# Kernel tuning notes

Hardware: AMD Instinct MI355X
Metric: run time of the kernel (lower is better)

Reference implementation:

```python
import jax, jax.numpy as jnp
import numpy as np

NUM_LEVELS = 16
BASE_RES = 16
DESIRED_RES = 512
EMBED_C = 2
LOG2_HASHMAP = 19
N_POINTS = 262144


def _level_params():
    # torch-ngp gridencoder math, align_corners=True
    S = np.log2(DESIRED_RES / BASE_RES) / (NUM_LEVELS - 1)
    scales = np.exp2(np.arange(NUM_LEVELS) * S) * BASE_RES - 1.0  # float per-level scale
    res = np.ceil(scales).astype(np.int64) + 1                     # per-level grid resolution
    sizes = np.minimum(res ** 3, 2 ** LOG2_HASHMAP)
    sizes = ((sizes + 7) // 8) * 8                                 # round up to multiple of 8
    offsets = np.concatenate([[0], np.cumsum(sizes)])
    return scales.astype(np.float32), res.astype(np.int32), offsets.astype(np.int32)


_CORNERS = np.array([[(c >> d) & 1 for d in range(3)] for c in range(8)], dtype=np.int32)  # [8,3]


def _grid_encode(x, table):
    # x: [N,3] in [0,1]; table: [total_entries, EMBED_C]
    scales, res, offsets = _level_params()
    scales_j = jnp.asarray(scales)[:, None, None]                    # [L,1,1]
    res_j = jnp.asarray(res)[:, None, None]                          # [L,1,1]
    hsize = jnp.asarray(offsets[1:] - offsets[:-1])[:, None, None]   # [L,1,1]
    off = jnp.asarray(offsets[:-1])[:, None, None]                   # [L,1,1]
    pos = x[None, :, :] * scales_j                                   # [L,N,3]
    pos_floor = jnp.floor(pos)
    frac = pos - pos_floor                                           # [L,N,3]
    base = pos_floor.astype(jnp.int32)                               # [L,N,3]
    stride = jnp.concatenate([jnp.ones_like(res_j), res_j, res_j * res_j], axis=-1)  # [L,1,3]
    corners = jnp.asarray(_CORNERS)                                  # [8,3]
    cg = base[:, :, None, :] + corners[None, None]                   # [L,N,8,3]
    w = jnp.where(corners[None, None].astype(bool), frac[:, :, None, :], 1.0 - frac[:, :, None, :])
    w = w[..., 0] * w[..., 1] * w[..., 2]                            # [L,N,8] trilinear weights
    lin = jnp.sum(cg * stride[:, :, None, :], axis=-1)               # [L,N,8] linear corner index
    idx = off + lin % hsize                                          # tiled gridtype: modulo, no hash
    feats = table[idx]                                               # [L,N,8,C] gather
    out = jnp.einsum('lnk,lnkc->lnc', w, feats)                      # [L,N,C]
    n = out.shape[1]
    return out.transpose(1, 0, 2).reshape(n, NUM_LEVELS * EMBED_C)   # [N, L*C]


def setup_inputs() -> dict:
    key = jax.random.key(0)
    ks = jax.random.split(key, 8)
    _, _, offsets = _level_params()
    total = int(offsets[-1])
    inputcoords = jax.random.uniform(ks[0], (N_POINTS, 1, 3), dtype=jnp.float32)  # in [0,1): (x+1)/2 stays in [0,1]
    embeddings = jax.random.normal(ks[1], (total, 1, EMBED_C), dtype=jnp.float32) * 1e-2
    d_in = NUM_LEVELS * EMBED_C  # 32
    W0 = jax.random.normal(ks[2], (d_in, 32), dtype=jnp.float32) / np.sqrt(d_in)
    b0 = jnp.zeros((32,), jnp.float32)
    W1 = jax.random.normal(ks[3], (32, 32), dtype=jnp.float32) / np.sqrt(32.0)
    b1 = jnp.zeros((32,), jnp.float32)
    W2 = jax.random.normal(ks[4], (32, 1), dtype=jnp.float32) / np.sqrt(32.0)
    b2 = jnp.zeros((1,), jnp.float32)
    return {"inputcoords": inputcoords, "embeddings": embeddings,
            "W0": W0, "b0": b0, "W1": W1, "b1": b1, "W2": W2, "b2": b2}


def reference(inputcoords, embeddings, W0, b0, W1, b1, W2, b2):
    bound = 1.0
    x = ((inputcoords + bound) / (2.0 * bound)).reshape(-1, 3)       # [N,3]
    enc = _grid_encode(x, embeddings[:, 0])                          # [N, 32]
    h = enc.reshape(-1, 1, NUM_LEVELS * EMBED_C)                     # [N,1,32]
    h = jax.nn.leaky_relu(h @ W0 + b0, 0.01)
    h = jax.nn.leaky_relu(h @ W1 + b1, 0.01)
    return h @ W2 + b2                                               # [N,1,1]
```

## Files before the change

kernel.cpp:

```cpp
#include <hip/hip_runtime.h>

#define NLVL 16

constexpr float SCALEC[NLVL] = {
    15.0f, 19.15873679831797f, 24.39841683149119f, 31.0f,
    39.31747359663594f, 49.79683366298238f, 63.0f, 79.63494719327189f,
    100.59366732596477f, 127.0f, 160.26989438654376f, 202.18733465192954f,
    255.0f, 321.5397887730875f, 405.3746693038591f, 511.0f
};
constexpr int RESC[NLVL] = {
    16, 21, 26, 32, 41, 51, 64, 81, 102, 128, 162, 204, 256, 323, 407, 512
};
constexpr int OFFC[NLVL] = {
    0, 4096, 13360, 30936, 63704, 132632, 265288, 527432,
    1051720, 1576008, 2100296, 2624584, 3148872, 3673160, 4197448, 4721736
};
constexpr int HMASK = 0x7FFFF;

template<int L>
__device__ __forceinline__ void lvl_issue(float x, float y, float z,
                                          const float* __restrict__ emb,
                                          float4& q0, float4& q1,
                                          float4& q2, float4& q3)
{
    constexpr float s  = SCALEC[L];
    constexpr int   r  = RESC[L];
    constexpr int   r2 = RESC[L] * RESC[L];
    constexpr int   off = OFFC[L];

    const float px = x * s, py = y * s, pz = z * s;
    const int lin = (int)floorf(px) + r * (int)floorf(py) + r2 * (int)floorf(pz);
    int i0 = lin, i1 = lin + r, i2 = lin + r2, i3 = lin + r2 + r;
    if constexpr (L >= 7) { i0 &= HMASK; i1 &= HMASK; i2 &= HMASK; i3 &= HMASK; }
    __builtin_memcpy(&q0, emb + 2 * (off + i0), 16);
    __builtin_memcpy(&q1, emb + 2 * (off + i1), 16);
    __builtin_memcpy(&q2, emb + 2 * (off + i2), 16);
    __builtin_memcpy(&q3, emb + 2 * (off + i3), 16);
}

template<int L>
__device__ __forceinline__ void lvl_finish(float x, float y, float z,
                                           const float* __restrict__ emb,
                                           float4 q0, float4 q1,
                                           float4 q2, float4 q3,
                                           float& a0, float& a1)
{
    constexpr float s  = SCALEC[L];
    constexpr int   r  = RESC[L];
    constexpr int   r2 = RESC[L] * RESC[L];
    constexpr int   off = OFFC[L];

    const float px = x * s, py = y * s, pz = z * s;
    const float tx = px - floorf(px), ty = py - floorf(py), tz = pz - floorf(pz);

    if constexpr (L >= 7) {
        const int lin = (int)floorf(px) + r * (int)floorf(py) + r2 * (int)floorf(pz);
        const int i0 = lin & HMASK, i1 = (lin + r) & HMASK;
        const int i2 = (lin + r2) & HMASK, i3 = (lin + r2 + r) & HMASK;
        const float f0x = emb[2 * off], f0y = emb[2 * off + 1];
        q0.z = (i0 == HMASK) ? f0x : q0.z;  q0.w = (i0 == HMASK) ? f0y : q0.w;
        q1.z = (i1 == HMASK) ? f0x : q1.z;  q1.w = (i1 == HMASK) ? f0y : q1.w;
        q2.z = (i2 == HMASK) ? f0x : q2.z;  q2.w = (i2 == HMASK) ? f0y : q2.w;
        q3.z = (i3 == HMASK) ? f0x : q3.z;  q3.w = (i3 == HMASK) ? f0y : q3.w;
    }

    const float wx1 = tx, wx0 = 1.0f - tx;
    const float wy1 = ty, wy0 = 1.0f - ty;
    const float wz1 = tz, wz0 = 1.0f - tz;
    const float w00 = wy0 * wz0, w10 = wy1 * wz0;
    const float w01 = wy0 * wz1, w11 = wy1 * wz1;
    float r0 = 0.0f, r1 = 0.0f;
    r0 = fmaf(w00 * wx0, q0.x, r0); r1 = fmaf(w00 * wx0, q0.y, r1);
    r0 = fmaf(w00 * wx1, q0.z, r0); r1 = fmaf(w00 * wx1, q0.w, r1);
    r0 = fmaf(w10 * wx0, q1.x, r0); r1 = fmaf(w10 * wx0, q1.y, r1);
    r0 = fmaf(w10 * wx1, q1.z, r0); r1 = fmaf(w10 * wx1, q1.w, r1);
    r0 = fmaf(w01 * wx0, q2.x, r0); r1 = fmaf(w01 * wx0, q2.y, r1);
    r0 = fmaf(w01 * wx1, q2.z, r0); r1 = fmaf(w01 * wx1, q2.w, r1);
    r0 = fmaf(w11 * wx0, q3.x, r0); r1 = fmaf(w11 * wx0, q3.y, r1);
    r0 = fmaf(w11 * wx1, q3.z, r0); r1 = fmaf(w11 * wx1, q3.w, r1);
    a0 = r0; a1 = r1;
}

template<int G>
__device__ __forceinline__ void enc_pair(int p, float x, float y, float z,
                                         const float* __restrict__ emb,
                                         float* __restrict__ ws, int n)
{
    constexpr int LA = G, LB = G + 8;
    float4 a0, a1, a2, a3, b0, b1, b2, b3;
    lvl_issue<LA>(x, y, z, emb, a0, a1, a2, a3);
    lvl_issue<LB>(x, y, z, emb, b0, b1, b2, b3);
    float ea0, ea1, eb0, eb1;
    lvl_finish<LA>(x, y, z, emb, a0, a1, a2, a3, ea0, ea1);
    lvl_finish<LB>(x, y, z, emb, b0, b1, b2, b3, eb0, eb1);
    ws[(size_t)(2 * LA + 0) * n + p] = ea0;
    ws[(size_t)(2 * LA + 1) * n + p] = ea1;
    ws[(size_t)(2 * LB + 0) * n + p] = eb0;
    ws[(size_t)(2 * LB + 1) * n + p] = eb1;
}

__global__ __launch_bounds__(256)
void enc_kernel(const float* __restrict__ coords,
                const float* __restrict__ emb,
                float* __restrict__ ws, int n)
{
    const int p = blockIdx.x * 256 + threadIdx.x;
    if (p >= n) return;
    const float x = (coords[p * 3 + 0] + 1.0f) * 0.5f;
    const float y = (coords[p * 3 + 1] + 1.0f) * 0.5f;
    const float z = (coords[p * 3 + 2] + 1.0f) * 0.5f;
    switch (blockIdx.y) {
        case 0: enc_pair<0>(p, x, y, z, emb, ws, n); break;
        case 1: enc_pair<1>(p, x, y, z, emb, ws, n); break;
        case 2: enc_pair<2>(p, x, y, z, emb, ws, n); break;
        case 3: enc_pair<3>(p, x, y, z, emb, ws, n); break;
        case 4: enc_pair<4>(p, x, y, z, emb, ws, n); break;
        case 5: enc_pair<5>(p, x, y, z, emb, ws, n); break;
        case 6: enc_pair<6>(p, x, y, z, emb, ws, n); break;
        default: enc_pair<7>(p, x, y, z, emb, ws, n); break;
    }
}

__global__ __launch_bounds__(256)
void mlp_kernel(const float* __restrict__ ws,
                const float* __restrict__ W0, const float* __restrict__ b0,
                const float* __restrict__ W1, const float* __restrict__ b1,
                const float* __restrict__ W2, const float* __restrict__ b2,
                float* __restrict__ out, int n)
{
    const int p = blockIdx.x * 256 + threadIdx.x;
    if (p >= n) return;

    float enc[32];
#pragma unroll
    for (int c = 0; c < 32; ++c) enc[c] = ws[(size_t)c * n + p];

    float h0[32];
#pragma unroll
    for (int j = 0; j < 32; ++j) h0[j] = b0[j];
#pragma unroll
    for (int i = 0; i < 32; ++i) {
        const float e = enc[i];
#pragma unroll
        for (int j = 0; j < 32; ++j) h0[j] = fmaf(e, W0[i * 32 + j], h0[j]);
    }
#pragma unroll
    for (int j = 0; j < 32; ++j) h0[j] = (h0[j] >= 0.0f) ? h0[j] : 0.01f * h0[j];

    float h1[32];
#pragma unroll
    for (int j = 0; j < 32; ++j) h1[j] = b1[j];
#pragma unroll
    for (int i = 0; i < 32; ++i) {
        const float e = h0[i];
#pragma unroll
        for (int j = 0; j < 32; ++j) h1[j] = fmaf(e, W1[i * 32 + j], h1[j]);
    }
#pragma unroll
    for (int j = 0; j < 32; ++j) h1[j] = (h1[j] >= 0.0f) ? h1[j] : 0.01f * h1[j];

    float acc = b2[0];
#pragma unroll
    for (int j = 0; j < 32; ++j) acc = fmaf(h1[j], W2[j], acc);

    out[p] = acc;
}

template<int L>
__device__ __forceinline__ void fuse_level(float x, float y, float z,
                                           const float* __restrict__ emb,
                                           float4 q0, float4 q1,
                                           float4 q2, float4 q3,
                                           float* __restrict__ h0,
                                           const float* __restrict__ W0)
{
    float a0, a1;
    lvl_finish<L>(x, y, z, emb, q0, q1, q2, q3, a0, a1);
#pragma unroll
    for (int j = 0; j < 32; ++j)
        h0[j] = fmaf(a0, W0[(2 * L + 0) * 32 + j], h0[j]);
#pragma unroll
    for (int j = 0; j < 32; ++j)
        h0[j] = fmaf(a1, W0[(2 * L + 1) * 32 + j], h0[j]);
}

__global__ __launch_bounds__(256, 4)
void fused_kernel(const float* __restrict__ coords,
                  const float* __restrict__ emb,
                  const float* __restrict__ W0, const float* __restrict__ b0,
                  const float* __restrict__ W1, const float* __restrict__ b1,
                  const float* __restrict__ W2, const float* __restrict__ b2,
                  float* __restrict__ out, int n)
{
    const int tid = blockIdx.x * blockDim.x + threadIdx.x;
    if (tid >= n) return;
    const float x = (coords[tid * 3 + 0] + 1.0f) * 0.5f;
    const float y = (coords[tid * 3 + 1] + 1.0f) * 0.5f;
    const float z = (coords[tid * 3 + 2] + 1.0f) * 0.5f;

    float h0[32];
#pragma unroll
    for (int j = 0; j < 32; ++j) h0[j] = b0[j];

    float4 a0, a1, a2, a3, b0r, b1r, b2r, b3r;
#define ISS_A(L) lvl_issue<L>(x, y, z, emb, a0, a1, a2, a3);
#define ISS_B(L) lvl_issue<L>(x, y, z, emb, b0r, b1r, b2r, b3r);
#define FUS_A(L) fuse_level<L>(x, y, z, emb, a0, a1, a2, a3, h0, W0);
#define FUS_B(L) fuse_level<L>(x, y, z, emb, b0r, b1r, b2r, b3r, h0, W0);
    ISS_A(0)
    ISS_B(1)  FUS_A(0)
    ISS_A(2)  FUS_B(1)
    ISS_B(3)  FUS_A(2)
    ISS_A(4)  FUS_B(3)
    ISS_B(5)  FUS_A(4)
    ISS_A(6)  FUS_B(5)
    ISS_B(7)  FUS_A(6)
    ISS_A(8)  FUS_B(7)
    ISS_B(9)  FUS_A(8)
    ISS_A(10) FUS_B(9)
    ISS_B(11) FUS_A(10)
    ISS_A(12) FUS_B(11)
    ISS_B(13) FUS_A(12)
    ISS_A(14) FUS_B(13)
    ISS_B(15) FUS_A(14)
    FUS_B(15)
#undef ISS_A
#undef ISS_B
#undef FUS_A
#undef FUS_B

#pragma unroll
    for (int j = 0; j < 32; ++j) h0[j] = (h0[j] >= 0.0f) ? h0[j] : 0.01f * h0[j];
    float h1[32];
#pragma unroll
    for (int j = 0; j < 32; ++j) h1[j] = b1[j];
#pragma unroll
    for (int i = 0; i < 32; ++i) {
        const float e = h0[i];
#pragma unroll
        for (int j = 0; j < 32; ++j) h1[j] = fmaf(e, W1[i * 32 + j], h1[j]);
    }
#pragma unroll
    for (int j = 0; j < 32; ++j) h1[j] = (h1[j] >= 0.0f) ? h1[j] : 0.01f * h1[j];
    float acc = b2[0];
#pragma unroll
    for (int j = 0; j < 32; ++j) acc = fmaf(h1[j], W2[j], acc);
    out[tid] = acc;
}

extern "C" void kernel_launch(void* const* d_in, const int* in_sizes, int n_in,
                              void* d_out, int out_size, void* d_ws, size_t ws_size,
                              hipStream_t stream) {
    const float* coords = (const float*)d_in[0];
    const float* emb    = (const float*)d_in[1];
    const float* W0     = (const float*)d_in[2];
    const float* b0     = (const float*)d_in[3];
    const float* W1     = (const float*)d_in[4];
    const float* b1     = (const float*)d_in[5];
    const float* W2     = (const float*)d_in[6];
    const float* b2     = (const float*)d_in[7];
    float* out = (float*)d_out;

    const int n = in_sizes[0] / 3;
    const int nb = (n + 255) / 256;
    const size_t need = (size_t)32 * (size_t)n * sizeof(float);

    if (ws_size >= need) {
        dim3 grid(nb, 8);
        enc_kernel<<<grid, 256, 0, stream>>>(coords, emb, (float*)d_ws, n);
        mlp_kernel<<<nb, 256, 0, stream>>>((const float*)d_ws,
                                           W0, b0, W1, b1, W2, b2, out, n);
    } else {
        fused_kernel<<<nb, 256, 0, stream>>>(coords, emb,
                                             W0, b0, W1, b1, W2, b2, out, n);
    }
}
```

Measured before the change: 95.20 us.

## Process two points per thread in encoder with inline-asm gathers and staged waits

The encoder kernel now handles two points per thread, issuing 16 dwordx4 gathers through inline asm and then consuming them in stages with explicit s_waitcnt vmcnt counters and sched barriers. The grid becomes 1D with the level pair interleaved in the low bits of blockIdx.x. The aim is more memory-level parallelism per wave for the random table gathers, so latency overlaps with interpolation math. In exchange it uses more VGPRs, which may lower occupancy, and the hand-written waitcnt sequence is fragile if the compiler inserts other vector memory operations.

```diff
diff --git a/kernel.cpp b/kernel.cpp
--- a/kernel.cpp
+++ b/kernel.cpp
@@ -1,4 +1,6 @@
 #include <hip/hip_runtime.h>
+
+typedef __attribute__((ext_vector_type(4))) float f32x4;
 
 #define NLVL 16
 
@@ -18,10 +20,10 @@
 constexpr int HMASK = 0x7FFFF;
 
 template<int L>
-__device__ __forceinline__ void lvl_issue(float x, float y, float z,
-                                          const float* __restrict__ emb,
-                                          float4& q0, float4& q1,
-                                          float4& q2, float4& q3)
+__device__ __forceinline__ void lvl_issue_asm(float x, float y, float z,
+                                              const float* __restrict__ emb,
+                                              f32x4& q0, f32x4& q1,
+                                              f32x4& q2, f32x4& q3)
 {
     constexpr float s  = SCALEC[L];
     constexpr int   r  = RESC[L];
@@ -32,17 +34,21 @@
     const int lin = (int)floorf(px) + r * (int)floorf(py) + r2 * (int)floorf(pz);
     int i0 = lin, i1 = lin + r, i2 = lin + r2, i3 = lin + r2 + r;
     if constexpr (L >= 7) { i0 &= HMASK; i1 &= HMASK; i2 &= HMASK; i3 &= HMASK; }
-    __builtin_memcpy(&q0, emb + 2 * (off + i0), 16);
-    __builtin_memcpy(&q1, emb + 2 * (off + i1), 16);
-    __builtin_memcpy(&q2, emb + 2 * (off + i2), 16);
-    __builtin_memcpy(&q3, emb + 2 * (off + i3), 16);
+    const float* p0 = emb + 2 * (off + i0);
+    const float* p1 = emb + 2 * (off + i1);
+    const float* p2 = emb + 2 * (off + i2);
+    const float* p3 = emb + 2 * (off + i3);
+    asm volatile("global_load_dwordx4 %0, %1, off" : "=v"(q0) : "v"(p0));
+    asm volatile("global_load_dwordx4 %0, %1, off" : "=v"(q1) : "v"(p1));
+    asm volatile("global_load_dwordx4 %0, %1, off" : "=v"(q2) : "v"(p2));
+    asm volatile("global_load_dwordx4 %0, %1, off" : "=v"(q3) : "v"(p3));
 }
 
 template<int L>
 __device__ __forceinline__ void lvl_finish(float x, float y, float z,
                                            const float* __restrict__ emb,
-                                           float4 q0, float4 q1,
-                                           float4 q2, float4 q3,
+                                           f32x4 q0, f32x4 q1,
+                                           f32x4 q2, f32x4 q3,
                                            float& a0, float& a1)
 {
     constexpr float s  = SCALEC[L];
@@ -82,21 +88,40 @@
 }
 
 template<int G>
-__device__ __forceinline__ void enc_pair(int p, float x, float y, float z,
-                                         const float* __restrict__ emb,
-                                         float* __restrict__ ws, int n)
+__device__ __forceinline__ void enc_pair2(int p0, int p1,
+                                          float x0, float y0, float z0,
+                                          float x1, float y1, float z1,
+                                          const float* __restrict__ emb,
+                                          float* __restrict__ ws, int n)
 {
     constexpr int LA = G, LB = G + 8;
-    float4 a0, a1, a2, a3, b0, b1, b2, b3;
-    lvl_issue<LA>(x, y, z, emb, a0, a1, a2, a3);
-    lvl_issue<LB>(x, y, z, emb, b0, b1, b2, b3);
-    float ea0, ea1, eb0, eb1;
-    lvl_finish<LA>(x, y, z, emb, a0, a1, a2, a3, ea0, ea1);
-    lvl_finish<LB>(x, y, z, emb, b0, b1, b2, b3, eb0, eb1);
-    ws[(size_t)(2 * LA + 0) * n + p] = ea0;
-    ws[(size_t)(2 * LA + 1) * n + p] = ea1;
-    ws[(size_t)(2 * LB + 0) * n + p] = eb0;
-    ws[(size_t)(2 * LB + 1) * n + p] = eb1;
+    f32x4 a0, a1, a2, a3, b0, b1, b2, b3;
+    f32x4 c0, c1, c2, c3, d0, d1, d2, d3;
+    lvl_issue_asm<LA>(x0, y0, z0, emb, a0, a1, a2, a3);
+    lvl_issue_asm<LB>(x0, y0, z0, emb, b0, b1, b2, b3);
+    lvl_issue_asm<LA>(x1, y1, z1, emb, c0, c1, c2, c3);
+    lvl_issue_asm<LB>(x1, y1, z1, emb, d0, d1, d2, d3);
+
+    float e0, e1;
+#define VMWAIT(N) asm volatile("s_waitcnt vmcnt(" #N ")" ::: "memory"); \
+                  __builtin_amdgcn_sched_barrier(0);
+    VMWAIT(12)
+    lvl_finish<LA>(x0, y0, z0, emb, a0, a1, a2, a3, e0, e1);
+    ws[(size_t)(2 * LA + 0) * n + p0] = e0;
+    ws[(size_t)(2 * LA + 1) * n + p0] = e1;
+    VMWAIT(8)
+    lvl_finish<LB>(x0, y0, z0, emb, b0, b1, b2, b3, e0, e1);
+    ws[(size_t)(2 * LB + 0) * n + p0] = e0;
+    ws[(size_t)(2 * LB + 1) * n + p0] = e1;
+    VMWAIT(4)
+    lvl_finish<LA>(x1, y1, z1, emb, c0, c1, c2, c3, e0, e1);
+    ws[(size_t)(2 * LA + 0) * n + p1] = e0;
+    ws[(size_t)(2 * LA + 1) * n + p1] = e1;
+    VMWAIT(0)
+    lvl_finish<LB>(x1, y1, z1, emb, d0, d1, d2, d3, e0, e1);
+    ws[(size_t)(2 * LB + 0) * n + p1] = e0;
+    ws[(size_t)(2 * LB + 1) * n + p1] = e1;
+#undef VMWAIT
 }
 
 __global__ __launch_bounds__(256)
@@ -104,20 +129,54 @@
                 const float* __restrict__ emb,
                 float* __restrict__ ws, int n)
 {
-    const int p = blockIdx.x * 256 + threadIdx.x;
-    if (p >= n) return;
-    const float x = (coords[p * 3 + 0] + 1.0f) * 0.5f;
-    const float y = (coords[p * 3 + 1] + 1.0f) * 0.5f;
-    const float z = (coords[p * 3 + 2] + 1.0f) * 0.5f;
-    switch (blockIdx.y) {
-        case 0: enc_pair<0>(p, x, y, z, emb, ws, n); break;
-        case 1: enc_pair<1>(p, x, y, z, emb, ws, n); break;
-        case 2: enc_pair<2>(p, x, y, z, emb, ws, n); break;
-        case 3: enc_pair<3>(p, x, y, z, emb, ws, n); break;
-        case 4: enc_pair<4>(p, x, y, z, emb, ws, n); break;
-        case 5: enc_pair<5>(p, x, y, z, emb, ws, n); break;
-        case 6: enc_pair<6>(p, x, y, z, emb, ws, n); break;
-        default: enc_pair<7>(p, x, y, z, emb, ws, n); break;
+    const int pair = blockIdx.x & 7;
+    const int pblk = blockIdx.x >> 3;
+    const int p0 = pblk * 512 + threadIdx.x;
+    const int p1 = p0 + 256;
+    if (p1 >= n) {
+        if (p0 >= n) return;
+        const float x = (coords[p0 * 3 + 0] + 1.0f) * 0.5f;
+        const float y = (coords[p0 * 3 + 1] + 1.0f) * 0.5f;
+        const float z = (coords[p0 * 3 + 2] + 1.0f) * 0.5f;
+        f32x4 a0, a1, a2, a3, b0, b1, b2, b3;
+        float e0, e1;
+        switch (pair) {
+#define CASE1(G) case G: { \
+            lvl_issue_asm<G>(x, y, z, emb, a0, a1, a2, a3); \
+            lvl_issue_asm<G + 8>(x, y, z, emb, b0, b1, b2, b3); \
+            asm volatile("s_waitcnt vmcnt(4)" ::: "memory"); \
+            __builtin_amdgcn_sched_barrier(0); \
+            lvl_finish<G>(x, y, z, emb, a0, a1, a2, a3, e0, e1); \
+            ws[(size_t)(2 * G + 0) * n + p0] = e0; \
+            ws[(size_t)(2 * G + 1) * n + p0] = e1; \
+            asm volatile("s_waitcnt vmcnt(0)" ::: "memory"); \
+            __builtin_amdgcn_sched_barrier(0); \
+            lvl_finish<G + 8>(x, y, z, emb, b0, b1, b2, b3, e0, e1); \
+            ws[(size_t)(2 * (G + 8) + 0) * n + p0] = e0; \
+            ws[(size_t)(2 * (G + 8) + 1) * n + p0] = e1; } break;
+            CASE1(0) CASE1(1) CASE1(2) CASE1(3)
+            CASE1(4) CASE1(5) CASE1(6) CASE1(7)
+#undef CASE1
+        }
+        return;
+    }
+
+    const float x0 = (coords[p0 * 3 + 0] + 1.0f) * 0.5f;
+    const float y0 = (coords[p0 * 3 + 1] + 1.0f) * 0.5f;
+    const float z0 = (coords[p0 * 3 + 2] + 1.0f) * 0.5f;
+    const float x1 = (coords[p1 * 3 + 0] + 1.0f) * 0.5f;
+    const float y1 = (coords[p1 * 3 + 1] + 1.0f) * 0.5f;
+    const float z1 = (coords[p1 * 3 + 2] + 1.0f) * 0.5f;
+
+    switch (pair) {
+        case 0: enc_pair2<0>(p0, p1, x0, y0, z0, x1, y1, z1, emb, ws, n); break;
+        case 1: enc_pair2<1>(p0, p1, x0, y0, z0, x1, y1, z1, emb, ws, n); break;
+        case 2: enc_pair2<2>(p0, p1, x0, y0, z0, x1, y1, z1, emb, ws, n); break;
+        case 3: enc_pair2<3>(p0, p1, x0, y0, z0, x1, y1, z1, emb, ws, n); break;
+        case 4: enc_pair2<4>(p0, p1, x0, y0, z0, x1, y1, z1, emb, ws, n); break;
+        case 5: enc_pair2<5>(p0, p1, x0, y0, z0, x1, y1, z1, emb, ws, n); break;
+        case 6: enc_pair2<6>(p0, p1, x0, y0, z0, x1, y1, z1, emb, ws, n); break;
+        default: enc_pair2<7>(p0, p1, x0, y0, z0, x1, y1, z1, emb, ws, n); break;
     }
 }
 
@@ -164,6 +223,30 @@
     for (int j = 0; j < 32; ++j) acc = fmaf(h1[j], W2[j], acc);
 
     out[p] = acc;
+}
+
+__device__ __forceinline__ void lvl_issue_c(int L_dummy, float, float, float,
+                                            const float*, float4&, float4&,
+                                            float4&, float4&) {}
+
+template<int L>
+__device__ __forceinline__ void lvl_issue(float x, float y, float z,
+                                          const float* __restrict__ emb,
+                                          float4& q0, float4& q1,
+                                          float4& q2, float4& q3)
+{
+    constexpr float s  = SCALEC[L];
+    constexpr int   r  = RESC[L];
+    constexpr int   r2 = RESC[L] * RESC[L];
+    constexpr int   off = OFFC[L];
+    const float px = x * s, py = y * s, pz = z * s;
+    const int lin = (int)floorf(px) + r * (int)floorf(py) + r2 * (int)floorf(pz);
+    int i0 = lin, i1 = lin + r, i2 = lin + r2, i3 = lin + r2 + r;
+    if constexpr (L >= 7) { i0 &= HMASK; i1 &= HMASK; i2 &= HMASK; i3 &= HMASK; }
+    __builtin_memcpy(&q0, emb + 2 * (off + i0), 16);
+    __builtin_memcpy(&q1, emb + 2 * (off + i1), 16);
+    __builtin_memcpy(&q2, emb + 2 * (off + i2), 16);
+    __builtin_memcpy(&q3, emb + 2 * (off + i3), 16);
 }
 
 template<int L>
@@ -174,8 +257,10 @@
                                            float* __restrict__ h0,
                                            const float* __restrict__ W0)
 {
+    f32x4 v0 = {q0.x, q0.y, q0.z, q0.w}, v1 = {q1.x, q1.y, q1.z, q1.w};
+    f32x4 v2 = {q2.x, q2.y, q2.z, q2.w}, v3 = {q3.x, q3.y, q3.z, q3.w};
     float a0, a1;
-    lvl_finish<L>(x, y, z, emb, q0, q1, q2, q3, a0, a1);
+    lvl_finish<L>(x, y, z, emb, v0, v1, v2, v3, a0, a1);
 #pragma unroll
     for (int j = 0; j < 32; ++j)
         h0[j] = fmaf(a0, W0[(2 * L + 0) * 32 + j], h0[j]);
@@ -262,15 +347,16 @@
     float* out = (float*)d_out;
 
     const int n = in_sizes[0] / 3;
-    const int nb = (n + 255) / 256;
     const size_t need = (size_t)32 * (size_t)n * sizeof(float);
 
     if (ws_size >= need) {
-        dim3 grid(nb, 8);
-        enc_kernel<<<grid, 256, 0, stream>>>(coords, emb, (float*)d_ws, n);
+        const int nb2 = (n + 511) / 512;
+        enc_kernel<<<nb2 * 8, 256, 0, stream>>>(coords, emb, (float*)d_ws, n);
+        const int nb = (n + 255) / 256;
         mlp_kernel<<<nb, 256, 0, stream>>>((const float*)d_ws,
                                            W0, b0, W1, b1, W2, b2, out, n);
     } else {
+        const int nb = (n + 255) / 256;
         fused_kernel<<<nb, 256, 0, stream>>>(coords, emb,
                                              W0, b0, W1, b1, W2, b2, out, n);
     }
```

After: 103.3 us. 1.08x slower.

## Use inline-asm gathers with split waitcnt, float4 workspace, and interleaved block order

Applied to the files above, without the earlier changes.

The encoder now issues the eight embedding gathers with inline global_load_dwordx4 asm and waits in two steps (vmcnt(4), then vmcnt(0)), so the first level's interpolation can start while the second level's loads are still in flight. The workspace layout changes to one float4 per (level-pair, point), which makes the encoder's four scalar stores one vector store and the MLP's 32 scalar loads eight vector loads. The grid becomes 1D with the level-pair index in the low bits of blockIdx.x, so blocks that read the same coordinates run close together in time. The asm loads rely on hand-placed waitcnts for correctness, and the sched_barriers limit how the compiler can schedule around them.

```diff
diff --git a/kernel.cpp b/kernel.cpp
--- a/kernel.cpp
+++ b/kernel.cpp
@@ -1,4 +1,6 @@
 #include <hip/hip_runtime.h>
+
+typedef __attribute__((ext_vector_type(4))) float f32x4;
 
 #define NLVL 16
 
@@ -18,10 +20,10 @@
 constexpr int HMASK = 0x7FFFF;
 
 template<int L>
-__device__ __forceinline__ void lvl_issue(float x, float y, float z,
-                                          const float* __restrict__ emb,
-                                          float4& q0, float4& q1,
-                                          float4& q2, float4& q3)
+__device__ __forceinline__ void lvl_issue_asm(float x, float y, float z,
+                                              const float* __restrict__ emb,
+                                              f32x4& q0, f32x4& q1,
+                                              f32x4& q2, f32x4& q3)
 {
     constexpr float s  = SCALEC[L];
     constexpr int   r  = RESC[L];
@@ -32,17 +34,21 @@
     const int lin = (int)floorf(px) + r * (int)floorf(py) + r2 * (int)floorf(pz);
     int i0 = lin, i1 = lin + r, i2 = lin + r2, i3 = lin + r2 + r;
     if constexpr (L >= 7) { i0 &= HMASK; i1 &= HMASK; i2 &= HMASK; i3 &= HMASK; }
-    __builtin_memcpy(&q0, emb + 2 * (off + i0), 16);
-    __builtin_memcpy(&q1, emb + 2 * (off + i1), 16);
-    __builtin_memcpy(&q2, emb + 2 * (off + i2), 16);
-    __builtin_memcpy(&q3, emb + 2 * (off + i3), 16);
+    const float* p0 = emb + 2 * (off + i0);
+    const float* p1 = emb + 2 * (off + i1);
+    const float* p2 = emb + 2 * (off + i2);
+    const float* p3 = emb + 2 * (off + i3);
+    asm volatile("global_load_dwordx4 %0, %1, off" : "=v"(q0) : "v"(p0));
+    asm volatile("global_load_dwordx4 %0, %1, off" : "=v"(q1) : "v"(p1));
+    asm volatile("global_load_dwordx4 %0, %1, off" : "=v"(q2) : "v"(p2));
+    asm volatile("global_load_dwordx4 %0, %1, off" : "=v"(q3) : "v"(p3));
 }
 
 template<int L>
 __device__ __forceinline__ void lvl_finish(float x, float y, float z,
                                            const float* __restrict__ emb,
-                                           float4 q0, float4 q1,
-                                           float4 q2, float4 q3,
+                                           f32x4 q0, f32x4 q1,
+                                           f32x4 q2, f32x4 q3,
                                            float& a0, float& a1)
 {
     constexpr float s  = SCALEC[L];
@@ -82,47 +88,53 @@
 }
 
 template<int G>
-__device__ __forceinline__ void enc_pair(int p, float x, float y, float z,
-                                         const float* __restrict__ emb,
-                                         float* __restrict__ ws, int n)
-{
-    constexpr int LA = G, LB = G + 8;
-    float4 a0, a1, a2, a3, b0, b1, b2, b3;
-    lvl_issue<LA>(x, y, z, emb, a0, a1, a2, a3);
-    lvl_issue<LB>(x, y, z, emb, b0, b1, b2, b3);
-    float ea0, ea1, eb0, eb1;
-    lvl_finish<LA>(x, y, z, emb, a0, a1, a2, a3, ea0, ea1);
-    lvl_finish<LB>(x, y, z, emb, b0, b1, b2, b3, eb0, eb1);
-    ws[(size_t)(2 * LA + 0) * n + p] = ea0;
-    ws[(size_t)(2 * LA + 1) * n + p] = ea1;
-    ws[(size_t)(2 * LB + 0) * n + p] = eb0;
-    ws[(size_t)(2 * LB + 1) * n + p] = eb1;
+__device__ __forceinline__ void enc_one(int p, float x, float y, float z,
+                                        const float* __restrict__ emb,
+                                        float4* __restrict__ ws, int n)
+{
+    f32x4 a0, a1, a2, a3, b0, b1, b2, b3;
+    lvl_issue_asm<G>(x, y, z, emb, a0, a1, a2, a3);
+    lvl_issue_asm<G + 8>(x, y, z, emb, b0, b1, b2, b3);
+
+    float e0, e1, e2, e3;
+    asm volatile("s_waitcnt vmcnt(4)" ::: "memory");
+    __builtin_amdgcn_sched_barrier(0);
+    lvl_finish<G>(x, y, z, emb, a0, a1, a2, a3, e0, e1);
+    asm volatile("s_waitcnt vmcnt(0)" ::: "memory");
+    __builtin_amdgcn_sched_barrier(0);
+    lvl_finish<G + 8>(x, y, z, emb, b0, b1, b2, b3, e2, e3);
+
+    const float4 v = {e0, e1, e2, e3};
+    ws[(size_t)G * n + p] = v;
 }
 
 __global__ __launch_bounds__(256)
 void enc_kernel(const float* __restrict__ coords,
                 const float* __restrict__ emb,
-                float* __restrict__ ws, int n)
-{
-    const int p = blockIdx.x * 256 + threadIdx.x;
+                float4* __restrict__ ws, int n)
+{
+    const int pair = blockIdx.x & 7;
+    const int p = (blockIdx.x >> 3) * 256 + threadIdx.x;
     if (p >= n) return;
+
     const float x = (coords[p * 3 + 0] + 1.0f) * 0.5f;
     const float y = (coords[p * 3 + 1] + 1.0f) * 0.5f;
     const float z = (coords[p * 3 + 2] + 1.0f) * 0.5f;
-    switch (blockIdx.y) {
-        case 0: enc_pair<0>(p, x, y, z, emb, ws, n); break;
-        case 1: enc_pair<1>(p, x, y, z, emb, ws, n); break;
-        case 2: enc_pair<2>(p, x, y, z, emb, ws, n); break;
-        case 3: enc_pair<3>(p, x, y, z, emb, ws, n); break;
-        case 4: enc_pair<4>(p, x, y, z, emb, ws, n); break;
-        case 5: enc_pair<5>(p, x, y, z, emb, ws, n); break;
-        case 6: enc_pair<6>(p, x, y, z, emb, ws, n); break;
-        default: enc_pair<7>(p, x, y, z, emb, ws, n); break;
+
+    switch (pair) {
+        case 0: enc_one<0>(p, x, y, z, emb, ws, n); break;
+        case 1: enc_one<1>(p, x, y, z, emb, ws, n); break;
+        case 2: enc_one<2>(p, x, y, z, emb, ws, n); break;
+        case 3: enc_one<3>(p, x, y, z, emb, ws, n); break;
+        case 4: enc_one<4>(p, x, y, z, emb, ws, n); break;
+        case 5: enc_one<5>(p, x, y, z, emb, ws, n); break;
+        case 6: enc_one<6>(p, x, y, z, emb, ws, n); break;
+        default: enc_one<7>(p, x, y, z, emb, ws, n); break;
     }
 }
 
 __global__ __launch_bounds__(256)
-void mlp_kernel(const float* __restrict__ ws,
+void mlp_kernel(const float4* __restrict__ ws,
                 const float* __restrict__ W0, const float* __restrict__ b0,
                 const float* __restrict__ W1, const float* __restrict__ b1,
                 const float* __restrict__ W2, const float* __restrict__ b2,
@@ -133,7 +145,13 @@
 
     float enc[32];
 #pragma unroll
-    for (int c = 0; c < 32; ++c) enc[c] = ws[(size_t)c * n + p];
+    for (int g = 0; g < 8; ++g) {
+        const float4 v = ws[(size_t)g * n + p];
+        enc[2 * g + 0]      = v.x;
+        enc[2 * g + 1]      = v.y;
+        enc[2 * (g + 8) + 0] = v.z;
+        enc[2 * (g + 8) + 1] = v.w;
+    }
 
     float h0[32];
 #pragma unroll
@@ -164,6 +182,26 @@
     for (int j = 0; j < 32; ++j) acc = fmaf(h1[j], W2[j], acc);
 
     out[p] = acc;
+}
+
+template<int L>
+__device__ __forceinline__ void lvl_issue(float x, float y, float z,
+                                          const float* __restrict__ emb,
+                                          float4& q0, float4& q1,
+                                          float4& q2, float4& q3)
+{
+    constexpr float s  = SCALEC[L];
+    constexpr int   r  = RESC[L];
+    constexpr int   r2 = RESC[L] * RESC[L];
+    constexpr int   off = OFFC[L];
+    const float px = x * s, py = y * s, pz = z * s;
+    const int lin = (int)floorf(px) + r * (int)floorf(py) + r2 * (int)floorf(pz);
+    int i0 = lin, i1 = lin + r, i2 = lin + r2, i3 = lin + r2 + r;
+    if constexpr (L >= 7) { i0 &= HMASK; i1 &= HMASK; i2 &= HMASK; i3 &= HMASK; }
+    __builtin_memcpy(&q0, emb + 2 * (off + i0), 16);
+    __builtin_memcpy(&q1, emb + 2 * (off + i1), 16);
+    __builtin_memcpy(&q2, emb + 2 * (off + i2), 16);
+    __builtin_memcpy(&q3, emb + 2 * (off + i3), 16);
 }
 
 template<int L>
@@ -174,8 +212,10 @@
                                            float* __restrict__ h0,
                                            const float* __restrict__ W0)
 {
+    f32x4 v0 = {q0.x, q0.y, q0.z, q0.w}, v1 = {q1.x, q1.y, q1.z, q1.w};
+    f32x4 v2 = {q2.x, q2.y, q2.z, q2.w}, v3 = {q3.x, q3.y, q3.z, q3.w};
     float a0, a1;
-    lvl_finish<L>(x, y, z, emb, q0, q1, q2, q3, a0, a1);
+    lvl_finish<L>(x, y, z, emb, v0, v1, v2, v3, a0, a1);
 #pragma unroll
     for (int j = 0; j < 32; ++j)
         h0[j] = fmaf(a0, W0[(2 * L + 0) * 32 + j], h0[j]);
@@ -263,12 +303,11 @@
 
     const int n = in_sizes[0] / 3;
     const int nb = (n + 255) / 256;
-    const size_t need = (size_t)32 * (size_t)n * sizeof(float);
+    const size_t need = (size_t)8 * (size_t)n * sizeof(float4);
 
     if (ws_size >= need) {
-        dim3 grid(nb, 8);
-        enc_kernel<<<grid, 256, 0, stream>>>(coords, emb, (float*)d_ws, n);
-        mlp_kernel<<<nb, 256, 0, stream>>>((const float*)d_ws,
+        enc_kernel<<<nb * 8, 256, 0, stream>>>(coords, emb, (float4*)d_ws, n);
+        mlp_kernel<<<nb, 256, 0, stream>>>((const float4*)d_ws,
                                            W0, b0, W1, b1, W2, b2, out, n);
     } else {
         fused_kernel<<<nb, 256, 0, stream>>>(coords, emb,
```

New measurement: 106.7 us. +12.1%, slower.

## Spatially sort points into Morton buckets before hash-grid encoding

Applied to the files above, without the earlier changes.

Adds a counting sort of the points into 32^3 Morton-ordered spatial buckets (zero, histogram, scan, scatter kernels), so that neighbouring threads in the encoding kernel gather nearby table entries and get better cache locality. The encoder now writes float4-packed level pairs and interleaves the pair index into blockIdx.x. The MLP scatters results back to the original point order. This costs four extra launches, atomics, and an extra read/write of the coordinates, and the single-block scan is serial.

```diff
diff --git a/kernel.cpp b/kernel.cpp
--- a/kernel.cpp
+++ b/kernel.cpp
@@ -17,6 +17,8 @@
 };
 constexpr int HMASK = 0x7FFFF;
 
+#define NBUCKET 32768
+
 template<int L>
 __device__ __forceinline__ void lvl_issue(float x, float y, float z,
                                           const float* __restrict__ emb,
@@ -27,7 +29,6 @@
     constexpr int   r  = RESC[L];
     constexpr int   r2 = RESC[L] * RESC[L];
     constexpr int   off = OFFC[L];
-
     const float px = x * s, py = y * s, pz = z * s;
     const int lin = (int)floorf(px) + r * (int)floorf(py) + r2 * (int)floorf(pz);
     int i0 = lin, i1 = lin + r, i2 = lin + r2, i3 = lin + r2 + r;
@@ -82,47 +83,134 @@
 }
 
 template<int G>
-__device__ __forceinline__ void enc_pair(int p, float x, float y, float z,
-                                         const float* __restrict__ emb,
-                                         float* __restrict__ ws, int n)
-{
-    constexpr int LA = G, LB = G + 8;
+__device__ __forceinline__ float4 enc_point(float x, float y, float z,
+                                            const float* __restrict__ emb)
+{
     float4 a0, a1, a2, a3, b0, b1, b2, b3;
-    lvl_issue<LA>(x, y, z, emb, a0, a1, a2, a3);
-    lvl_issue<LB>(x, y, z, emb, b0, b1, b2, b3);
-    float ea0, ea1, eb0, eb1;
-    lvl_finish<LA>(x, y, z, emb, a0, a1, a2, a3, ea0, ea1);
-    lvl_finish<LB>(x, y, z, emb, b0, b1, b2, b3, eb0, eb1);
-    ws[(size_t)(2 * LA + 0) * n + p] = ea0;
-    ws[(size_t)(2 * LA + 1) * n + p] = ea1;
-    ws[(size_t)(2 * LB + 0) * n + p] = eb0;
-    ws[(size_t)(2 * LB + 1) * n + p] = eb1;
-}
-
-__global__ __launch_bounds__(256)
-void enc_kernel(const float* __restrict__ coords,
-                const float* __restrict__ emb,
-                float* __restrict__ ws, int n)
+    lvl_issue<G>(x, y, z, emb, a0, a1, a2, a3);
+    lvl_issue<G + 8>(x, y, z, emb, b0, b1, b2, b3);
+    float e0, e1, e2, e3;
+    lvl_finish<G>(x, y, z, emb, a0, a1, a2, a3, e0, e1);
+    lvl_finish<G + 8>(x, y, z, emb, b0, b1, b2, b3, e2, e3);
+    return make_float4(e0, e1, e2, e3);
+}
+
+__device__ __forceinline__ int bucket_key(float x, float y, float z)
+{
+    int kx = (int)((x * 2.0f - 1.0f) * 32.0f);
+    int ky = (int)((y * 2.0f - 1.0f) * 32.0f);
+    int kz = (int)((z * 2.0f - 1.0f) * 32.0f);
+    kx = min(31, max(0, kx)); ky = min(31, max(0, ky)); kz = min(31, max(0, kz));
+    int m = 0;
+#pragma unroll
+    for (int b = 0; b < 5; ++b) {
+        m |= (((kx >> b) & 1) << (3 * b))
+           | (((ky >> b) & 1) << (3 * b + 1))
+           | (((kz >> b) & 1) << (3 * b + 2));
+    }
+    return m;
+}
+
+__global__ __launch_bounds__(256)
+void zero_kernel(int* __restrict__ counts)
+{
+    const int i = blockIdx.x * 256 + threadIdx.x;
+    if (i < NBUCKET) counts[i] = 0;
+}
+
+__global__ __launch_bounds__(256)
+void hist_kernel(const float* __restrict__ coords, int* __restrict__ counts, int n)
 {
     const int p = blockIdx.x * 256 + threadIdx.x;
     if (p >= n) return;
     const float x = (coords[p * 3 + 0] + 1.0f) * 0.5f;
     const float y = (coords[p * 3 + 1] + 1.0f) * 0.5f;
     const float z = (coords[p * 3 + 2] + 1.0f) * 0.5f;
-    switch (blockIdx.y) {
-        case 0: enc_pair<0>(p, x, y, z, emb, ws, n); break;
-        case 1: enc_pair<1>(p, x, y, z, emb, ws, n); break;
-        case 2: enc_pair<2>(p, x, y, z, emb, ws, n); break;
-        case 3: enc_pair<3>(p, x, y, z, emb, ws, n); break;
-        case 4: enc_pair<4>(p, x, y, z, emb, ws, n); break;
-        case 5: enc_pair<5>(p, x, y, z, emb, ws, n); break;
-        case 6: enc_pair<6>(p, x, y, z, emb, ws, n); break;
-        default: enc_pair<7>(p, x, y, z, emb, ws, n); break;
-    }
-}
-
-__global__ __launch_bounds__(256)
-void mlp_kernel(const float* __restrict__ ws,
+    atomicAdd(&counts[bucket_key(x, y, z)], 1);
+}
+
+__global__ __launch_bounds__(1024)
+void scan_kernel(const int* __restrict__ counts, int* __restrict__ offsets)
+{
+    __shared__ int part[1024];
+    const int t = threadIdx.x;
+    const int base = t * (NBUCKET / 1024);
+    int sum = 0;
+#pragma unroll
+    for (int i = 0; i < NBUCKET / 1024; ++i) sum += counts[base + i];
+    part[t] = sum;
+    __syncthreads();
+    for (int s = 1; s < 1024; s <<= 1) {
+        const int v = (t >= s) ? part[t - s] : 0;
+        __syncthreads();
+        part[t] += v;
+        __syncthreads();
+    }
+    int run = part[t] - sum;
+#pragma unroll
+    for (int i = 0; i < NBUCKET / 1024; ++i) {
+        offsets[base + i] = run;
+        run += counts[base + i];
+    }
+}
+
+__global__ __launch_bounds__(256)
+void scatter_kernel(const float* __restrict__ coords, int* __restrict__ offsets,
+                    float4* __restrict__ sc, int n)
+{
+    const int p = blockIdx.x * 256 + threadIdx.x;
+    if (p >= n) return;
+    const float x = (coords[p * 3 + 0] + 1.0f) * 0.5f;
+    const float y = (coords[p * 3 + 1] + 1.0f) * 0.5f;
+    const float z = (coords[p * 3 + 2] + 1.0f) * 0.5f;
+    const int dst = atomicAdd(&offsets[bucket_key(x, y, z)], 1);
+    sc[dst] = make_float4(x, y, z, __int_as_float(p));
+}
+
+__global__ __launch_bounds__(256)
+void enc_sorted(const float4* __restrict__ sc, const float* __restrict__ emb,
+                float4* __restrict__ encws, int n)
+{
+    const int pair = blockIdx.x & 7;
+    const int q = (blockIdx.x >> 3) * 256 + threadIdx.x;
+    if (q >= n) return;
+    const float4 c = sc[q];
+    switch (pair) {
+        case 0: encws[(size_t)0 * n + q] = enc_point<0>(c.x, c.y, c.z, emb); break;
+        case 1: encws[(size_t)1 * n + q] = enc_point<1>(c.x, c.y, c.z, emb); break;
+        case 2: encws[(size_t)2 * n + q] = enc_point<2>(c.x, c.y, c.z, emb); break;
+        case 3: encws[(size_t)3 * n + q] = enc_point<3>(c.x, c.y, c.z, emb); break;
+        case 4: encws[(size_t)4 * n + q] = enc_point<4>(c.x, c.y, c.z, emb); break;
+        case 5: encws[(size_t)5 * n + q] = enc_point<5>(c.x, c.y, c.z, emb); break;
+        case 6: encws[(size_t)6 * n + q] = enc_point<6>(c.x, c.y, c.z, emb); break;
+        default: encws[(size_t)7 * n + q] = enc_point<7>(c.x, c.y, c.z, emb); break;
+    }
+}
+
+__global__ __launch_bounds__(256)
+void enc_unsorted(const float* __restrict__ coords, const float* __restrict__ emb,
+                  float4* __restrict__ encws, int n)
+{
+    const int pair = blockIdx.x & 7;
+    const int q = (blockIdx.x >> 3) * 256 + threadIdx.x;
+    if (q >= n) return;
+    const float x = (coords[q * 3 + 0] + 1.0f) * 0.5f;
+    const float y = (coords[q * 3 + 1] + 1.0f) * 0.5f;
+    const float z = (coords[q * 3 + 2] + 1.0f) * 0.5f;
+    switch (pair) {
+        case 0: encws[(size_t)0 * n + q] = enc_point<0>(x, y, z, emb); break;
+        case 1: encws[(size_t)1 * n + q] = enc_point<1>(x, y, z, emb); break;
+        case 2: encws[(size_t)2 * n + q] = enc_point<2>(x, y, z, emb); break;
+        case 3: encws[(size_t)3 * n + q] = enc_point<3>(x, y, z, emb); break;
+        case 4: encws[(size_t)4 * n + q] = enc_point<4>(x, y, z, emb); break;
+        case 5: encws[(size_t)5 * n + q] = enc_point<5>(x, y, z, emb); break;
+        case 6: encws[(size_t)6 * n + q] = enc_point<6>(x, y, z, emb); break;
+        default: encws[(size_t)7 * n + q] = enc_point<7>(x, y, z, emb); break;
+    }
+}
+
+__global__ __launch_bounds__(256)
+void mlp_kernel(const float4* __restrict__ encws, const float4* __restrict__ sc,
                 const float* __restrict__ W0, const float* __restrict__ b0,
                 const float* __restrict__ W1, const float* __restrict__ b1,
                 const float* __restrict__ W2, const float* __restrict__ b2,
@@ -133,7 +221,13 @@
 
     float enc[32];
 #pragma unroll
-    for (int c = 0; c < 32; ++c) enc[c] = ws[(size_t)c * n + p];
+    for (int g = 0; g < 8; ++g) {
+        const float4 v = encws[(size_t)g * n + p];
+        enc[2 * g + 0]       = v.x;
+        enc[2 * g + 1]       = v.y;
+        enc[2 * (g + 8) + 0] = v.z;
+        enc[2 * (g + 8) + 1] = v.w;
+    }
 
     float h0[32];
 #pragma unroll
@@ -163,7 +257,8 @@
 #pragma unroll
     for (int j = 0; j < 32; ++j) acc = fmaf(h1[j], W2[j], acc);
 
-    out[p] = acc;
+    const int o = sc ? __float_as_int(sc[p].w) : p;
+    out[o] = acc;
 }
 
 template<int L>
@@ -263,12 +358,29 @@
 
     const int n = in_sizes[0] / 3;
     const int nb = (n + 255) / 256;
-    const size_t need = (size_t)32 * (size_t)n * sizeof(float);
-
-    if (ws_size >= need) {
-        dim3 grid(nb, 8);
-        enc_kernel<<<grid, 256, 0, stream>>>(coords, emb, (float*)d_ws, n);
-        mlp_kernel<<<nb, 256, 0, stream>>>((const float*)d_ws,
+
+    char* base = (char*)d_ws;
+    int*    counts  = (int*)base;
+    int*    offsets = (int*)(base + NBUCKET * 4);
+    float4* sc      = (float4*)(base + 2 * (size_t)NBUCKET * 4);
+    float4* encws   = (float4*)(base + 2 * (size_t)NBUCKET * 4 + (size_t)n * 16);
+
+    const size_t need_sorted = 2 * (size_t)NBUCKET * 4 + (size_t)n * 16
+                             + (size_t)n * 128;
+    const size_t need_plain  = (size_t)n * 128;
+
+    if (ws_size >= need_sorted) {
+        zero_kernel<<<(NBUCKET + 255) / 256, 256, 0, stream>>>(counts);
+        hist_kernel<<<nb, 256, 0, stream>>>(coords, counts, n);
+        scan_kernel<<<1, 1024, 0, stream>>>(counts, offsets);
+        scatter_kernel<<<nb, 256, 0, stream>>>(coords, offsets, sc, n);
+        enc_sorted<<<nb * 8, 256, 0, stream>>>(sc, emb, encws, n);
+        mlp_kernel<<<nb, 256, 0, stream>>>(encws, sc,
+                                           W0, b0, W1, b1, W2, b2, out, n);
+    } else if (ws_size >= need_plain) {
+        float4* encp = (float4*)d_ws;
+        enc_unsorted<<<nb * 8, 256, 0, stream>>>(coords, emb, encp, n);
+        mlp_kernel<<<nb, 256, 0, stream>>>(encp, nullptr,
                                            W0, b0, W1, b1, W2, b2, out, n);
     } else {
         fused_kernel<<<nb, 256, 0, stream>>>(coords, emb,
```

New measurement: 150.3 us. +57.9%, slower.
